# Optimization experiments

Measured on AMD Instinct MI355X. Metric: run time of the kernel, lower is better.

Reference implementation:

```python
import jax, jax.numpy as jnp
import numpy as np

B, H, L, D = 2, 16, 2048, 64
P = 2            # pos_dim
F = D // 2       # rotation pairs
MIN_FREQ, MAX_FREQ = 0.5, 40.0


def setup_inputs() -> dict:
    key = jax.random.key(0)
    kq, kk, kv, kf = jax.random.split(key, 4)
    query = jax.random.normal(kq, (B, H, L, D), dtype=jnp.float32)
    key_t = jax.random.normal(kk, (B, H, L, D), dtype=jnp.float32)
    value = jax.random.normal(kv, (B, H, L, D), dtype=jnp.float32)
    # default positions per _ensure_pos: arange(L) broadcast to [B, L, P]
    pos = jnp.broadcast_to(jnp.arange(L, dtype=jnp.float32)[None, :, None], (B, L, P))
    # normalize to [0,1) grid-like coords as typical for 2D RoPE in diffusion
    pos = pos / jnp.float32(L)
    # golden-gate-style freqs: log-spaced magnitudes x random unit directions, per head
    mags = jnp.exp(jnp.linspace(jnp.log(MIN_FREQ), jnp.log(MAX_FREQ), F, dtype=jnp.float32))  # [F]
    dirs = jax.random.normal(kf, (H, F, P), dtype=jnp.float32)
    dirs = dirs / jnp.linalg.norm(dirs, axis=-1, keepdims=True)
    freqs_hfp = dirs * (2.0 * jnp.pi * mags)[None, :, None]  # [H, F, P]
    return {"query": query, "key": key_t, "value": value, "pos": pos, "freqs_hfp": freqs_hfp}


def _apply_rope(x, theta):
    # x: [B,H,L,D], theta: [B,H,L,F]; rotate-half convention (first/second halves paired)
    x1, x2 = x[..., :F], x[..., F:]
    c, s = jnp.cos(theta), jnp.sin(theta)
    return jnp.concatenate([x1 * c - x2 * s, x2 * c + x1 * s], axis=-1)


def reference(query, key, value, pos, freqs_hfp):
    # RoPE angles: contract positions against per-head freq directions
    theta = jnp.einsum("blp,hfp->bhlf", pos, freqs_hfp)  # [B,H,L,F]
    q_rot = _apply_rope(query, theta)
    k_rot = _apply_rope(key, theta)
    # FlexAttention with noop score_mod == standard scaled softmax attention
    scale = 1.0 / jnp.sqrt(jnp.float32(D))
    scores = jnp.einsum("bhld,bhmd->bhlm", q_rot, k_rot) * scale  # [B,H,L,L]
    probs = jax.nn.softmax(scores, axis=-1)
    out = jnp.einsum("bhlm,bhmd->bhld", probs, value)
    return out
```

## Files before the change

kernel.cpp:

```cpp
#include <hip/hip_runtime.h>
#include <math.h>

constexpr int B_ = 2, H_ = 16, L_ = 2048, D_ = 64, F_ = 32;
constexpr int BH_ = B_ * H_;
constexpr float SCALE_LOG2E = 0.125f * 1.44269504088896340736f;
constexpr float INV_2PI = 0.15915494309189535f;

using half8   = __attribute__((ext_vector_type(8))) _Float16;
using floatx16 = __attribute__((ext_vector_type(16))) float;
using uint2v  = __attribute__((ext_vector_type(2))) unsigned int;
typedef unsigned int u32;

__device__ inline float fexp2(float x) { return __builtin_amdgcn_exp2f(x); }

__global__ __launch_bounds__(256) void rope_v_prepass(
    const float* __restrict__ q, const float* __restrict__ k,
    const float* __restrict__ v, const float* __restrict__ pos,
    const float* __restrict__ freqs,
    _Float16* __restrict__ qr, _Float16* __restrict__ kr,
    _Float16* __restrict__ vt) {
  __shared__ _Float16 vls[64][66];

  const int tid  = threadIdx.x;
  const int r0   = blockIdx.x * 64;
  const int lrow = tid >> 2;
  const int j    = tid & 3;
  const int row  = r0 + lrow;
  const int l    = row % L_;
  const int h    = (row / L_) % H_;
  const int b    = row / (H_ * L_);

  const float p0 = pos[(b * L_ + l) * 2 + 0];
  const float p1 = pos[(b * L_ + l) * 2 + 1];

  float c[8], s[8];
  #pragma unroll
  for (int i = 0; i < 8; ++i) {
    const int f = j * 8 + i;
    const float th = p0 * freqs[(h * F_ + f) * 2 + 0] +
                     p1 * freqs[(h * F_ + f) * 2 + 1];
    float t = th * INV_2PI;
    t -= rintf(t);
    c[i] = __builtin_amdgcn_cosf(t);
    s[i] = __builtin_amdgcn_sinf(t);
  }

  const float* qrow = q + (size_t)row * D_;
  const float* krow = k + (size_t)row * D_;

  {
    float x1[8], x2[8];
    *(float4*)(x1)     = *(const float4*)(qrow + j * 8);
    *(float4*)(x1 + 4) = *(const float4*)(qrow + j * 8 + 4);
    *(float4*)(x2)     = *(const float4*)(qrow + j * 8 + 32);
    *(float4*)(x2 + 4) = *(const float4*)(qrow + j * 8 + 36);
    half8 o1, o2;
    #pragma unroll
    for (int i = 0; i < 8; ++i) {
      o1[i] = (_Float16)((x1[i] * c[i] - x2[i] * s[i]) * SCALE_LOG2E);
      o2[i] = (_Float16)((x2[i] * c[i] + x1[i] * s[i]) * SCALE_LOG2E);
    }
    *(half8*)(qr + (size_t)row * D_ + j * 8)      = o1;
    *(half8*)(qr + (size_t)row * D_ + 32 + j * 8) = o2;
  }
  {
    float x1[8], x2[8];
    *(float4*)(x1)     = *(const float4*)(krow + j * 8);
    *(float4*)(x1 + 4) = *(const float4*)(krow + j * 8 + 4);
    *(float4*)(x2)     = *(const float4*)(krow + j * 8 + 32);
    *(float4*)(x2 + 4) = *(const float4*)(krow + j * 8 + 36);
    half8 o1, o2;
    #pragma unroll
    for (int i = 0; i < 8; ++i) {
      o1[i] = (_Float16)(x1[i] * c[i] - x2[i] * s[i]);
      o2[i] = (_Float16)(x2[i] * c[i] + x1[i] * s[i]);
    }
    *(half8*)(kr + (size_t)row * D_ + j * 8)      = o1;
    *(half8*)(kr + (size_t)row * D_ + 32 + j * 8) = o2;
  }

  const float* vrow = v + (size_t)row * D_;
  #pragma unroll
  for (int i4 = 0; i4 < 4; ++i4) {
    float4 vv = *(const float4*)(vrow + j * 16 + i4 * 4);
    vls[lrow][j * 16 + i4 * 4 + 0] = (_Float16)vv.x;
    vls[lrow][j * 16 + i4 * 4 + 1] = (_Float16)vv.y;
    vls[lrow][j * 16 + i4 * 4 + 2] = (_Float16)vv.z;
    vls[lrow][j * 16 + i4 * 4 + 3] = (_Float16)vv.w;
  }
  __syncthreads();
  const int d  = tid >> 2;
  const int jj = tid & 3;
  const int bh = b * H_ + h;
  half8 w0, w1;
  #pragma unroll
  for (int i = 0; i < 8; ++i) {
    w0[i] = vls[jj * 16 + i][d];
    w1[i] = vls[jj * 16 + 8 + i][d];
  }
  const size_t vtoff = ((size_t)bh * D_ + d) * L_ + (size_t)(r0 % L_) + jj * 16;
  *(half8*)(vt + vtoff)     = w0;
  *(half8*)(vt + vtoff + 8) = w1;
}

__global__ __launch_bounds__(256, 2) void flash_attn(
    const _Float16* __restrict__ qr, const _Float16* __restrict__ kr,
    const _Float16* __restrict__ vt, float* __restrict__ out) {
  __shared__ _Float16 Kl[128 * 64];
  __shared__ _Float16 Vl[64 * 128];

  const int bid  = blockIdx.x;
  const int wg   = (bid & 7) * 64 + (bid >> 3);
  const int head = wg >> 4;
  const int qb   = wg & 15;

  const int tid  = threadIdx.x;
  const int wid  = tid >> 6;
  const int lane = tid & 63;
  const int ql   = lane & 31;
  const int hi   = lane >> 5;

  const _Float16* qbase =
      qr + ((size_t)head * L_ + (size_t)(qb * 128 + wid * 32 + ql)) * D_;
  half8 qf[4];
  #pragma unroll
  for (int c = 0; c < 4; ++c) qf[c] = *(const half8*)(qbase + c * 16 + hi * 8);

  floatx16 o0 = {}, o1 = {};
  float m = -1.0e4f, lsum = 0.f;

  const _Float16* kb = kr + (size_t)head * L_ * D_;
  const _Float16* vb = vt + (size_t)head * D_ * L_;

  int koff[4], voff[8];
  #pragma unroll
  for (int c = 0; c < 4; ++c)
    koff[c] = (ql * 128 + c * 32 + hi * 16) ^ ((ql & 7) << 4);
  #pragma unroll
  for (int kc = 0; kc < 8; ++kc)
    voff[kc] = (ql * 256 + kc * 32 + hi * 16) ^ ((ql & 15) << 4);

  constexpr int NT = L_ / 128;

  for (int t = 0; t < NT; ++t) {
    __syncthreads();
    #pragma unroll
    for (int ci = 0; ci < 4; ++ci) {
      const int c = tid + ci * 256;
      const int krw = c >> 3, kcc = c & 7, kcd = kcc ^ (krw & 7);
      const uint4 dk =
          *(const uint4*)(kb + (size_t)(t * 128 + krw) * D_ + kcd * 8);
      *(uint4*)((char*)Kl + krw * 128 + kcc * 16) = dk;
      const int vrw = c >> 4, vcc = c & 15, vcd = vcc ^ (vrw & 15);
      const uint4 dv =
          *(const uint4*)(vb + (size_t)vrw * L_ + t * 128 + vcd * 8);
      *(uint4*)((char*)Vl + vrw * 256 + vcc * 16) = dv;
    }
    __syncthreads();

    floatx16 s0 = {}, s1 = {}, s2 = {}, s3 = {};
    #pragma unroll
    for (int c = 0; c < 4; ++c) {
      const half8 k0 = *(const half8*)((const char*)Kl + koff[c]);
      const half8 k1 = *(const half8*)((const char*)Kl + koff[c] + 4096);
      const half8 k2 = *(const half8*)((const char*)Kl + koff[c] + 8192);
      const half8 k3 = *(const half8*)((const char*)Kl + koff[c] + 12288);
      s0 = __builtin_amdgcn_mfma_f32_32x32x16_f16(k0, qf[c], s0, 0, 0, 0);
      s1 = __builtin_amdgcn_mfma_f32_32x32x16_f16(k1, qf[c], s1, 0, 0, 0);
      s2 = __builtin_amdgcn_mfma_f32_32x32x16_f16(k2, qf[c], s2, 0, 0, 0);
      s3 = __builtin_amdgcn_mfma_f32_32x32x16_f16(k3, qf[c], s3, 0, 0, 0);
    }

    float mx[16];
    #pragma unroll
    for (int r = 0; r < 16; ++r)
      mx[r] = fmaxf(fmaxf(s0[r], s1[r]), fmaxf(s2[r], s3[r]));
    #pragma unroll
    for (int st = 8; st > 0; st >>= 1)
      #pragma unroll
      for (int r = 0; r < 8; ++r)
        if (r < st) mx[r] = fmaxf(mx[r], mx[r + st]);
    float pm = mx[0];
    pm = fmaxf(pm, __shfl_xor(pm, 32));

    if (!__all(pm <= m + 8.f)) {
      const float mn  = fmaxf(m, pm);
      const float fac = fexp2(m - mn);
      lsum *= fac;
      #pragma unroll
      for (int r = 0; r < 16; ++r) { o0[r] *= fac; o1[r] *= fac; }
      m = mn;
    }

    float sm[16];
    #pragma unroll
    for (int r = 0; r < 16; ++r) {
      s0[r] = fexp2(s0[r] - m);
      s1[r] = fexp2(s1[r] - m);
      s2[r] = fexp2(s2[r] - m);
      s3[r] = fexp2(s3[r] - m);
      sm[r] = (s0[r] + s1[r]) + (s2[r] + s3[r]);
    }
    #pragma unroll
    for (int st = 8; st > 0; st >>= 1)
      #pragma unroll
      for (int r = 0; r < 8; ++r)
        if (r < st) sm[r] += sm[r + st];
    float rs = sm[0];
    rs += __shfl_xor(rs, 32);
    lsum += rs;

    u32 w[4][8];
    #pragma unroll
    for (int u = 0; u < 8; ++u) {
      w[0][u] = __builtin_bit_cast(u32,
                  __builtin_amdgcn_cvt_pkrtz(s0[2 * u], s0[2 * u + 1]));
      w[1][u] = __builtin_bit_cast(u32,
                  __builtin_amdgcn_cvt_pkrtz(s1[2 * u], s1[2 * u + 1]));
      w[2][u] = __builtin_bit_cast(u32,
                  __builtin_amdgcn_cvt_pkrtz(s2[2 * u], s2[2 * u + 1]));
      w[3][u] = __builtin_bit_cast(u32,
                  __builtin_amdgcn_cvt_pkrtz(s3[2 * u], s3[2 * u + 1]));
    }

    #pragma unroll
    for (int tt = 0; tt < 4; ++tt) {
      #pragma unroll
      for (int kcl = 0; kcl < 2; ++kcl) {
        const uint2v ra = __builtin_amdgcn_permlane32_swap(
            w[tt][4 * kcl + 0], w[tt][4 * kcl + 2], false, false);
        const uint2v rb = __builtin_amdgcn_permlane32_swap(
            w[tt][4 * kcl + 1], w[tt][4 * kcl + 3], false, false);
        uint4 bfw; bfw.x = ra.x; bfw.y = rb.x; bfw.z = ra.y; bfw.w = rb.y;
        const half8 pf = __builtin_bit_cast(half8, bfw);
        const int kc = tt * 2 + kcl;
        const half8 v0 = *(const half8*)((const char*)Vl + voff[kc]);
        const half8 v1 = *(const half8*)((const char*)Vl + voff[kc] + 8192);
        o0 = __builtin_amdgcn_mfma_f32_32x32x16_f16(v0, pf, o0, 0, 0, 0);
        o1 = __builtin_amdgcn_mfma_f32_32x32x16_f16(v1, pf, o1, 0, 0, 0);
      }
    }
  }

  const float inv = 1.0f / lsum;
  float* ob = out + ((size_t)head * L_ + (size_t)(qb * 128 + wid * 32 + ql)) * D_;
  #pragma unroll
  for (int b = 0; b < 4; ++b) {
    float4 v0, v1;
    v0.x = o0[4 * b + 0] * inv; v0.y = o0[4 * b + 1] * inv;
    v0.z = o0[4 * b + 2] * inv; v0.w = o0[4 * b + 3] * inv;
    v1.x = o1[4 * b + 0] * inv; v1.y = o1[4 * b + 1] * inv;
    v1.z = o1[4 * b + 2] * inv; v1.w = o1[4 * b + 3] * inv;
    *(float4*)(ob + 8 * b + 4 * hi)      = v0;
    *(float4*)(ob + 32 + 8 * b + 4 * hi) = v1;
  }
}

extern "C" void kernel_launch(void* const* d_in, const int* in_sizes, int n_in,
                              void* d_out, int out_size, void* d_ws, size_t ws_size,
                              hipStream_t stream) {
  const float* q     = (const float*)d_in[0];
  const float* k     = (const float*)d_in[1];
  const float* v     = (const float*)d_in[2];
  const float* pos   = (const float*)d_in[3];
  const float* freqs = (const float*)d_in[4];
  float* out = (float*)d_out;

  _Float16* qr = (_Float16*)d_ws;
  _Float16* kr = qr + (size_t)BH_ * L_ * D_;
  _Float16* vt = kr + (size_t)BH_ * L_ * D_;

  const int rows = B_ * H_ * L_;
  rope_v_prepass<<<rows / 64, 256, 0, stream>>>(q, k, v, pos, freqs, qr, kr, vt);

  const int nwg = BH_ * (L_ / 128);
  flash_attn<<<nwg, 256, 0, stream>>>(qr, kr, vt, out);
}
```

Baseline: 68.49 us.

## Double-buffer K/V tiles in LDS with register prefetch of next tile

Adds a second LDS buffer for K and V tiles and issues the global loads for the next tile into registers before computing on the current tile. After the PV MMAs the prefetched registers are written to the alternate buffer, leaving one barrier per iteration instead of two. The aim is to hide global-memory latency behind the MFMA work. In exchange, LDS use doubles to 64KB per block and register pressure rises from the 8 uint4 prefetch registers, which may cut occupancy below the 2 blocks per CU requested in launch bounds.

```diff
diff --git a/kernel.cpp b/kernel.cpp
--- a/kernel.cpp
+++ b/kernel.cpp
@@ -106,8 +106,8 @@
 __global__ __launch_bounds__(256, 2) void flash_attn(
     const _Float16* __restrict__ qr, const _Float16* __restrict__ kr,
     const _Float16* __restrict__ vt, float* __restrict__ out) {
-  __shared__ _Float16 Kl[128 * 64];
-  __shared__ _Float16 Vl[64 * 128];
+  __shared__ _Float16 Kl[2][128 * 64];
+  __shared__ _Float16 Vl[2][64 * 128];
 
   const int bid  = blockIdx.x;
   const int wg   = (bid & 7) * 64 + (bid >> 3);
@@ -142,29 +142,54 @@
 
   constexpr int NT = L_ / 128;
 
-  for (int t = 0; t < NT; ++t) {
-    __syncthreads();
+  {
+    uint4 kreg[4], vreg[4];
     #pragma unroll
     for (int ci = 0; ci < 4; ++ci) {
       const int c = tid + ci * 256;
       const int krw = c >> 3, kcc = c & 7, kcd = kcc ^ (krw & 7);
-      const uint4 dk =
-          *(const uint4*)(kb + (size_t)(t * 128 + krw) * D_ + kcd * 8);
-      *(uint4*)((char*)Kl + krw * 128 + kcc * 16) = dk;
+      kreg[ci] = *(const uint4*)(kb + (size_t)krw * D_ + kcd * 8);
       const int vrw = c >> 4, vcc = c & 15, vcd = vcc ^ (vrw & 15);
-      const uint4 dv =
-          *(const uint4*)(vb + (size_t)vrw * L_ + t * 128 + vcd * 8);
-      *(uint4*)((char*)Vl + vrw * 256 + vcc * 16) = dv;
-    }
-    __syncthreads();
+      vreg[ci] = *(const uint4*)(vb + (size_t)vrw * L_ + vcd * 8);
+    }
+    #pragma unroll
+    for (int ci = 0; ci < 4; ++ci) {
+      const int c = tid + ci * 256;
+      const int krw = c >> 3, kcc = c & 7;
+      *(uint4*)((char*)&Kl[0][0] + krw * 128 + kcc * 16) = kreg[ci];
+      const int vrw = c >> 4, vcc = c & 15;
+      *(uint4*)((char*)&Vl[0][0] + vrw * 256 + vcc * 16) = vreg[ci];
+    }
+  }
+  __syncthreads();
+
+  for (int t = 0; t < NT; ++t) {
+    const int cur = t & 1;
+
+    uint4 kreg[4], vreg[4];
+    if (t + 1 < NT) {
+      #pragma unroll
+      for (int ci = 0; ci < 4; ++ci) {
+        const int c = tid + ci * 256;
+        const int krw = c >> 3, kcc = c & 7, kcd = kcc ^ (krw & 7);
+        kreg[ci] =
+            *(const uint4*)(kb + (size_t)((t + 1) * 128 + krw) * D_ + kcd * 8);
+        const int vrw = c >> 4, vcc = c & 15, vcd = vcc ^ (vrw & 15);
+        vreg[ci] =
+            *(const uint4*)(vb + (size_t)vrw * L_ + (t + 1) * 128 + vcd * 8);
+      }
+    }
+
+    const char* kbuf = (const char*)&Kl[cur][0];
+    const char* vbuf = (const char*)&Vl[cur][0];
 
     floatx16 s0 = {}, s1 = {}, s2 = {}, s3 = {};
     #pragma unroll
     for (int c = 0; c < 4; ++c) {
-      const half8 k0 = *(const half8*)((const char*)Kl + koff[c]);
-      const half8 k1 = *(const half8*)((const char*)Kl + koff[c] + 4096);
-      const half8 k2 = *(const half8*)((const char*)Kl + koff[c] + 8192);
-      const half8 k3 = *(const half8*)((const char*)Kl + koff[c] + 12288);
+      const half8 k0 = *(const half8*)(kbuf + koff[c]);
+      const half8 k1 = *(const half8*)(kbuf + koff[c] + 4096);
+      const half8 k2 = *(const half8*)(kbuf + koff[c] + 8192);
+      const half8 k3 = *(const half8*)(kbuf + koff[c] + 12288);
       s0 = __builtin_amdgcn_mfma_f32_32x32x16_f16(k0, qf[c], s0, 0, 0, 0);
       s1 = __builtin_amdgcn_mfma_f32_32x32x16_f16(k1, qf[c], s1, 0, 0, 0);
       s2 = __builtin_amdgcn_mfma_f32_32x32x16_f16(k2, qf[c], s2, 0, 0, 0);
@@ -234,12 +259,26 @@
         uint4 bfw; bfw.x = ra.x; bfw.y = rb.x; bfw.z = ra.y; bfw.w = rb.y;
         const half8 pf = __builtin_bit_cast(half8, bfw);
         const int kc = tt * 2 + kcl;
-        const half8 v0 = *(const half8*)((const char*)Vl + voff[kc]);
-        const half8 v1 = *(const half8*)((const char*)Vl + voff[kc] + 8192);
+        const half8 v0 = *(const half8*)(vbuf + voff[kc]);
+        const half8 v1 = *(const half8*)(vbuf + voff[kc] + 8192);
         o0 = __builtin_amdgcn_mfma_f32_32x32x16_f16(v0, pf, o0, 0, 0, 0);
         o1 = __builtin_amdgcn_mfma_f32_32x32x16_f16(v1, pf, o1, 0, 0, 0);
       }
     }
+
+    if (t + 1 < NT) {
+      char* kn = (char*)&Kl[cur ^ 1][0];
+      char* vn = (char*)&Vl[cur ^ 1][0];
+      #pragma unroll
+      for (int ci = 0; ci < 4; ++ci) {
+        const int c = tid + ci * 256;
+        const int krw = c >> 3, kcc = c & 7;
+        *(uint4*)(kn + krw * 128 + kcc * 16) = kreg[ci];
+        const int vrw = c >> 4, vcc = c & 15;
+        *(uint4*)(vn + vrw * 256 + vcc * 16) = vreg[ci];
+      }
+    }
+    __syncthreads();
   }
 
   const float inv = 1.0f / lsum;
```

Result: no change. 69.22 us (+1.1%).
